# Optimization experiments

Measured on AMD Instinct MI355X. Metric: run time of the kernel, lower is better.

## Reference

```python
import jax, jax.numpy as jnp
import numpy as np

NUM_EMBEDDINGS = 8192
EMBEDDING_DIM = 512
COMMITMENT_COST = 0.25
DECAY = 0.99
EPSILON = 1e-05


def setup_inputs() -> dict:
    key = jax.random.key(0)
    k1, k2, k3, k4 = jax.random.split(key, 4)
    z = jax.random.normal(k1, (16, 2048, EMBEDDING_DIM), dtype=jnp.float32)
    weight = jax.random.normal(k2, (NUM_EMBEDDINGS, EMBEDDING_DIM), dtype=jnp.float32)
    ema_cluster_size = jax.random.uniform(k3, (NUM_EMBEDDINGS,), dtype=jnp.float32)
    ema_w = jax.random.normal(k4, (NUM_EMBEDDINGS, EMBEDDING_DIM), dtype=jnp.float32)
    return {"z": z, "weight": weight, "ema_cluster_size": ema_cluster_size, "ema_w": ema_w}


def reference(z, weight, ema_cluster_size, ema_w):
    K, D = weight.shape
    z_flat = z.reshape(-1, D)                                   # [N, D]
    # squared-distance matrix via expanded GEMM (same math as torch)
    dist = ((z_flat ** 2).sum(1, keepdims=True)
            + (weight ** 2).sum(1)
            - 2.0 * z_flat @ weight.T)                          # [N, K]
    codes = jnp.argmin(dist, axis=1)                            # [N]
    # training-mode EMA update: one-hot sums expressed as segment_sum
    counts = jax.ops.segment_sum(jnp.ones(z_flat.shape[0], dtype=z.dtype), codes, num_segments=K)
    dw = jax.ops.segment_sum(z_flat, codes, num_segments=K)     # encodings.T @ z_flat
    new_cs = ema_cluster_size * DECAY + (1.0 - DECAY) * counts
    new_ema_w = ema_w * DECAY + (1.0 - DECAY) * dw
    n = new_cs.sum()
    cluster_size = (new_cs + EPSILON) / (n + K * EPSILON) * n
    new_weight = new_ema_w / cluster_size[:, None]              # updated codebook
    z_q = new_weight[codes].reshape(z.shape)                    # lookup with UPDATED weights
    vq_loss = COMMITMENT_COST * jnp.mean((jax.lax.stop_gradient(z_q) - z) ** 2)
    z_q_out = z + jax.lax.stop_gradient(z_q - z)                # straight-through estimator
    codes_out = codes.reshape(z.shape[0], -1)
    return vq_loss, z_q_out, codes_out, new_weight, new_cs, new_ema_w
```

## Files before the change

kernel.cpp:

```cpp
#include <hip/hip_runtime.h>
#include <cstdint>

#define K_CODES 8192
#define D_DIM   512
#define N_VEC   32768
#define DECAY   0.99f
#define EPS_VQ  1e-5f
#define COMMIT  0.25f
#define MARGIN  0.25f

typedef _Float16 half_t;
typedef _Float16 half8 __attribute__((ext_vector_type(8)));
typedef _Float16 half4 __attribute__((ext_vector_type(4)));
typedef float    f32x4 __attribute__((ext_vector_type(4)));
typedef unsigned long long u64;

#define GL2L(g, l)                                                              \
    __builtin_amdgcn_global_load_lds(                                           \
        (const __attribute__((address_space(1))) unsigned int*)(g),             \
        (__attribute__((address_space(3))) unsigned int*)(l), 16, 0, 0)

__device__ __forceinline__ unsigned ordf(float f) {
    unsigned u = __float_as_uint(f);
    return (u & 0x80000000u) ? ~u : (u | 0x80000000u);
}
__device__ __forceinline__ float unordf(unsigned u) {
    u = (u & 0x80000000u) ? (u & 0x7FFFFFFFu) : ~u;
    return __uint_as_float(u);
}


__global__ __launch_bounds__(256)
void conv_half_kernel(const float* __restrict__ x, half_t* __restrict__ out) {
    int i = blockIdx.x * 256 + threadIdx.x;
    float4 v = ((const float4*)x)[i];
    half4 h = { (_Float16)v.x, (_Float16)v.y, (_Float16)v.z, (_Float16)v.w };
    *(half4*)(out + (size_t)i * 4) = h;
}

__global__ __launch_bounds__(256)
void wsq_kernel(const float* __restrict__ w, float* __restrict__ wsq) {
    int wave = threadIdx.x >> 6, lane = threadIdx.x & 63;
    int row  = blockIdx.x * 4 + wave;
    const float4* p = (const float4*)(w + (size_t)row * D_DIM);
    float4 a = p[lane], b = p[lane + 64];
    float s = a.x*a.x + a.y*a.y + a.z*a.z + a.w*a.w
            + b.x*b.x + b.y*b.y + b.z*b.z + b.w*b.w;
    #pragma unroll
    for (int off = 32; off; off >>= 1) s += __shfl_down(s, off);
    if (lane == 0) wsq[row] = s;
}

__global__ __launch_bounds__(256)
void dist1_kernel(const half_t* __restrict__ A, const half_t* __restrict__ B,
                  const float* __restrict__ wsq, uint4* __restrict__ partial) {
    __shared__ __align__(16) half_t As[128 * 64];
    __shared__ __align__(16) half_t Bs[128 * 64];

    const int k0 = blockIdx.x * 128;
    const int n0 = blockIdx.y * 128;
    const int t    = threadIdx.x;
    const int lane = t & 63;
    const int wave = t >> 6;
    const int wm = (wave >> 1) * 64;
    const int wn = (wave & 1) * 64;
    const int l15 = lane & 15;
    const int q   = lane >> 4;

    f32x4 acc[4][4];
    #pragma unroll
    for (int mi = 0; mi < 4; ++mi)
        #pragma unroll
        for (int ni = 0; ni < 4; ++ni) acc[mi][ni] = (f32x4)0.0f;

    for (int c = 0; c < 8; ++c) {
        const int koff = c * 64;
        #pragma unroll
        for (int it = 0; it < 4; ++it) {
            int idx  = t + 256 * it;
            int row  = idx >> 3;
            int col8 = (idx & 7) ^ (row & 7);
            GL2L(A + (size_t)(n0 + row) * D_DIM + koff + col8 * 8, As + idx * 8);
            GL2L(B + (size_t)(k0 + row) * D_DIM + koff + col8 * 8, Bs + idx * 8);
        }
        __syncthreads();
        #pragma unroll
        for (int kk = 0; kk < 2; ++kk) {
            half8 af[4], bf[4];
            const int cpos = ((kk * 4 + q) ^ (l15 & 7)) * 8;
            #pragma unroll
            for (int mi = 0; mi < 4; ++mi)
                af[mi] = *(const half8*)&As[(wm + mi * 16 + l15) * 64 + cpos];
            #pragma unroll
            for (int ni = 0; ni < 4; ++ni)
                bf[ni] = *(const half8*)&Bs[(wn + ni * 16 + l15) * 64 + cpos];
            #pragma unroll
            for (int mi = 0; mi < 4; ++mi)
                #pragma unroll
                for (int ni = 0; ni < 4; ++ni)
                    acc[mi][ni] = __builtin_amdgcn_mfma_f32_16x16x32_f16(
                        af[mi], bf[ni], acc[mi][ni], 0, 0, 0);
        }
        __syncthreads();
    }

    u64* sm = (u64*)As;
    #pragma unroll
    for (int mi = 0; mi < 4; ++mi) {
        #pragma unroll
        for (int r = 0; r < 4; ++r) {
            u64 k1 = ~0ull, k2 = ~0ull;
            #pragma unroll
            for (int ni = 0; ni < 4; ++ni) {
                int col = k0 + wn + ni * 16 + l15;
                float d = wsq[col] - 2.0f * acc[mi][ni][r];
                u64 key = ((u64)ordf(d) << 32) | (unsigned)col;
                if (key < k1) { k2 = k1; k1 = key; }
                else if (key < k2) k2 = key;
            }
            #pragma unroll
            for (int m = 1; m <= 8; m <<= 1) {
                u64 o1 = __shfl_xor(k1, m);
                u64 o2 = __shfl_xor(k2, m);
                u64 lo = k1 < o1 ? k1 : o1;
                u64 hi = k1 < o1 ? o1 : k1;
                u64 m2 = k2 < o2 ? k2 : o2;
                k1 = lo;
                k2 = m2 < hi ? m2 : hi;
            }
            if (l15 == 0) {
                int rl = wm + mi * 16 + q * 4 + r;
                int h  = wave & 1;
                sm[h * 256 + 2 * rl]     = k1;
                sm[h * 256 + 2 * rl + 1] = k2;
            }
        }
    }
    __syncthreads();
    if (t < 128) {
        u64 a1 = sm[2*t], a2 = sm[2*t + 1];
        u64 b1 = sm[256 + 2*t], b2 = sm[256 + 2*t + 1];
        u64 lo = a1 < b1 ? a1 : b1;
        u64 hi = a1 < b1 ? b1 : a1;
        u64 m2 = a2 < b2 ? a2 : b2;
        m2 = m2 < hi ? m2 : hi;
        partial[(size_t)blockIdx.x * N_VEC + n0 + t] =
            make_uint4((unsigned)lo, (unsigned)(lo >> 32),
                       (unsigned)(m2 >> 32), 0u);
    }
}

__global__ __launch_bounds__(256)
void reduce_top2_kernel(const uint4* __restrict__ partial,
                        int* __restrict__ codes_i, float* __restrict__ codes_f,
                        int* __restrict__ cnt, int* __restrict__ list) {
    int row = blockIdx.x * 256 + threadIdx.x;
    u64 k1 = ~0ull, k2 = ~0ull;
    unsigned vm2 = 0xFFFFFFFFu;
    for (int kb = 0; kb < 64; ++kb) {
        uint4 e = partial[(size_t)kb * N_VEC + row];
        u64 k = ((u64)e.y << 32) | e.x;
        if (k < k1) { k2 = k1; k1 = k; }
        else if (k < k2) k2 = k;
        vm2 = min(vm2, e.z);
    }
    unsigned so = min((unsigned)(k2 >> 32), vm2);
    float bv = unordf((unsigned)(k1 >> 32));
    float sv = unordf(so);
    int code = (int)(k1 & 0xFFFFFFFFu);
    codes_i[row] = code;
    codes_f[row] = (float)code;
    if (sv - bv < MARGIN) { int p = atomicAdd(cnt, 1); list[p] = row; }
}

__global__ __launch_bounds__(256)
void refine2_kernel(const float* __restrict__ z, const float* __restrict__ w,
                    const float* __restrict__ wsq,
                    const int* __restrict__ cnt, const int* __restrict__ list,
                    u64* __restrict__ exact) {
    __shared__ float zs[64][68];
    __shared__ float ws[64][68];
    __shared__ int rows_s[64];
    const int n  = *cnt;
    const int c0 = blockIdx.x * 64;
    const int t  = threadIdx.x;
    const int lr = t & 63, lc = t >> 6;
    const int ty = t >> 4, tx = t & 15;

    for (int row0 = blockIdx.y * 64; row0 < n; row0 += gridDim.y * 64) {
        if (t < 64) {
            int ri = row0 + t;
            rows_s[t] = list[ri < n ? ri : n - 1];
        }
        __syncthreads();
        float acc[4][4] = {};
        const int zrow = rows_s[lr];
        for (int k0 = 0; k0 < D_DIM; k0 += 64) {
            #pragma unroll
            for (int it = 0; it < 4; ++it) {
                int kc = (lc * 4 + it) * 4;
                float4 v = *(const float4*)(z + (size_t)zrow * D_DIM + k0 + kc);
                zs[kc+0][lr] = v.x; zs[kc+1][lr] = v.y;
                zs[kc+2][lr] = v.z; zs[kc+3][lr] = v.w;
                float4 u = *(const float4*)(w + (size_t)(c0 + lr) * D_DIM + k0 + kc);
                ws[kc+0][lr] = u.x; ws[kc+1][lr] = u.y;
                ws[kc+2][lr] = u.z; ws[kc+3][lr] = u.w;
            }
            __syncthreads();
            #pragma unroll 8
            for (int k = 0; k < 64; ++k) {
                float4 za = *(const float4*)&zs[k][ty * 4];
                float4 wa = *(const float4*)&ws[k][tx * 4];
                float zav[4] = {za.x, za.y, za.z, za.w};
                float wav[4] = {wa.x, wa.y, wa.z, wa.w};
                #pragma unroll
                for (int i = 0; i < 4; ++i)
                    #pragma unroll
                    for (int j = 0; j < 4; ++j)
                        acc[i][j] += zav[i] * wav[j];
            }
            __syncthreads();
        }
        #pragma unroll
        for (int i = 0; i < 4; ++i) {
            u64 key = ~0ull;
            #pragma unroll
            for (int j = 0; j < 4; ++j) {
                int c = c0 + tx * 4 + j;
                float d = wsq[c] - 2.0f * acc[i][j];
                u64 k = ((u64)ordf(d) << 32) | (unsigned)c;
                if (k < key) key = k;
            }
            #pragma unroll
            for (int m = 1; m <= 8; m <<= 1) {
                u64 o = __shfl_xor(key, m);
                key = o < key ? o : key;
            }
            if (tx == 0) atomicMin(exact + rows_s[ty * 4 + i], key);
        }
        __syncthreads();
    }
}

__global__ __launch_bounds__(256)
void refine_fix_kernel(const int* __restrict__ cnt, const int* __restrict__ list,
                       const u64* __restrict__ exact,
                       int* __restrict__ codes_i, float* __restrict__ codes_f) {
    int n = *cnt;
    for (int i = blockIdx.x * 256 + threadIdx.x; i < n; i += 64 * 256) {
        int row = list[i];
        int code = (int)(exact[row] & 0xFFFFFFFFu);
        codes_i[row] = code;
        codes_f[row] = (float)code;
    }
}

__global__ __launch_bounds__(256)
void scatter_kernel(const int* __restrict__ codes_i, const float* __restrict__ z,
                    float* __restrict__ cnt_acc, float* __restrict__ dw_acc) {
    int row = blockIdx.x * 8 + (threadIdx.x >> 5);
    int c   = threadIdx.x & 31;
    int code = codes_i[row];
    if (c == 0) atomicAdd(&cnt_acc[code], 1.0f);
    const float* zr = z + (size_t)row * D_DIM;
    float* dr = dw_acc + (size_t)code * D_DIM;
    #pragma unroll
    for (int d = c; d < D_DIM; d += 32) atomicAdd(&dr[d], zr[d]);
}

__global__ __launch_bounds__(256)
void cs_kernel(const float* __restrict__ ema_cs, float* __restrict__ cs_out,
               float* __restrict__ nsum) {
    __shared__ float wsum[4];
    int i = blockIdx.x * 256 + threadIdx.x;
    float v = ema_cs[i] * DECAY + (1.0f - DECAY) * cs_out[i];
    cs_out[i] = v;
    float s = v;
    #pragma unroll
    for (int off = 32; off; off >>= 1) s += __shfl_down(s, off);
    int lane = threadIdx.x & 63, wid = threadIdx.x >> 6;
    if (lane == 0) wsum[wid] = s;
    __syncthreads();
    if (threadIdx.x == 0)
        atomicAdd(nsum, wsum[0] + wsum[1] + wsum[2] + wsum[3]);
}

__global__ __launch_bounds__(256)
void weight_kernel(const float* __restrict__ ema_w, const float* __restrict__ cs,
                   const float* __restrict__ nsum_p,
                   float* __restrict__ emaw_out, float* __restrict__ w_out) {
    int i = blockIdx.x * 256 + threadIdx.x;
    float dw = emaw_out[i];
    float ne = ema_w[i] * DECAY + (1.0f - DECAY) * dw;
    emaw_out[i] = ne;
    int k = i >> 9;
    float n = *nsum_p;
    float csize = (cs[k] + EPS_VQ) / (n + (float)K_CODES * EPS_VQ) * n;
    w_out[i] = ne / csize;
}

__global__ __launch_bounds__(256)
void gather_loss_kernel(const float* __restrict__ z, const int* __restrict__ codes,
                        const float* __restrict__ w, float* __restrict__ zq,
                        float* __restrict__ loss_acc) {
    __shared__ float wsum[4];
    int row  = blockIdx.x * 4 + (threadIdx.x >> 6);
    int lane = threadIdx.x & 63;
    int code = codes[row];
    const float* zr = z + (size_t)row * D_DIM;
    const float* wr = w + (size_t)code * D_DIM;
    float s = 0.0f;
    #pragma unroll
    for (int d = lane; d < D_DIM; d += 64) {
        float qv = wr[d];
        float diff = qv - zr[d];
        s += diff * diff;
        zq[(size_t)row * D_DIM + d] = qv;
    }
    #pragma unroll
    for (int off = 32; off; off >>= 1) s += __shfl_down(s, off);
    int wid = threadIdx.x >> 6;
    if (lane == 0) wsum[wid] = s;
    __syncthreads();
    if (threadIdx.x == 0)
        atomicAdd(loss_acc, wsum[0] + wsum[1] + wsum[2] + wsum[3]);
}

__global__ void finalize_kernel(const float* __restrict__ loss_acc,
                                float* __restrict__ out0) {
    *out0 = COMMIT * (*loss_acc) / 16777216.0f;
}

extern "C" void kernel_launch(void* const* d_in, const int* in_sizes, int n_in,
                              void* d_out, int out_size, void* d_ws, size_t ws_size,
                              hipStream_t stream) {
    const float* z      = (const float*)d_in[0];
    const float* weight = (const float*)d_in[1];
    const float* ema_cs = (const float*)d_in[2];
    const float* ema_w  = (const float*)d_in[3];

    float* out       = (float*)d_out;
    float* out_loss  = out;
    float* out_zq    = out + 1;
    float* out_codes = out + 16777217;
    float* out_w     = out + 16809985;
    float* out_cs    = out + 21004289;
    float* out_emaw  = out + 21012481;

    half_t* A_hi = (half_t*)(out + 4);
    half_t* B_hi = (half_t*)(out + 8388612);
    uint4*  partial = (uint4*)(out + 16809988);

    char* ws = (char*)d_ws;
    float* wsq      = (float*)ws;
    int*   codes_i  = (int*)(ws + 32768);
    int*   cnt      = (int*)(ws + 163840);
    float* nsum     = (float*)(ws + 163844);
    float* loss_acc = (float*)(ws + 163848);
    int*   list     = (int*)(ws + 163856);
    u64*   exact    = (u64*)(ws + 294928);

    hipMemsetAsync(cnt, 0, 16, stream);
    hipMemsetAsync(exact, 0xFF, N_VEC * 8, stream);

    conv_half_kernel<<<N_VEC * D_DIM / 1024, 256, 0, stream>>>(z, A_hi);
    conv_half_kernel<<<K_CODES * D_DIM / 1024, 256, 0, stream>>>(weight, B_hi);
    wsq_kernel<<<K_CODES / 4, 256, 0, stream>>>(weight, wsq);

    dim3 g2(K_CODES / 128, N_VEC / 128);
    dist1_kernel<<<g2, 256, 0, stream>>>(A_hi, B_hi, wsq, partial);

    reduce_top2_kernel<<<N_VEC / 256, 256, 0, stream>>>(partial, codes_i,
                                                        out_codes, cnt, list);

    hipMemsetAsync(out_cs, 0, 8192 * 4, stream);
    hipMemsetAsync(out_emaw, 0, (size_t)4194304 * 4, stream);

    dim3 gr(K_CODES / 64, 64);
    refine2_kernel<<<gr, 256, 0, stream>>>(z, weight, wsq, cnt, list, exact);
    refine_fix_kernel<<<64, 256, 0, stream>>>(cnt, list, exact,
                                              codes_i, out_codes);

    scatter_kernel<<<N_VEC / 8, 256, 0, stream>>>(codes_i, z, out_cs, out_emaw);
    cs_kernel<<<K_CODES / 256, 256, 0, stream>>>(ema_cs, out_cs, nsum);
    weight_kernel<<<4194304 / 256, 256, 0, stream>>>(ema_w, out_cs, nsum,
                                                     out_emaw, out_w);
    gather_loss_kernel<<<N_VEC / 4, 256, 0, stream>>>(z, codes_i, out_w,
                                                      out_zq, loss_acc);
    finalize_kernel<<<1, 1, 0, stream>>>(loss_acc, out_loss);
}
```

Baseline: 1.081 ms.

## Replace 64-bit key shuffle top-2 reduction with float LDS transpose reduction

The dist1 epilogue now tracks the top-2 as float scores (acc - wsq/2, maximised) with a column index, rather than packed 64-bit ordered keys reduced via shuffles. Per-lane partials go to padded LDS, then each lane reduces a full row serially before the two column halves are merged. This removes 64-bit compares and cross-lane shuffles from the epilogue at the cost of more LDS traffic and an extra barrier. Tie-breaking on equal distances no longer prefers the lower index, and the score is rescaled, so second-best margins may differ slightly.

```diff
diff --git a/kernel.cpp b/kernel.cpp
--- a/kernel.cpp
+++ b/kernel.cpp
@@ -54,8 +54,9 @@
 __global__ __launch_bounds__(256)
 void dist1_kernel(const half_t* __restrict__ A, const half_t* __restrict__ B,
                   const float* __restrict__ wsq, uint4* __restrict__ partial) {
-    __shared__ __align__(16) half_t As[128 * 64];
-    __shared__ __align__(16) half_t Bs[128 * 64];
+    __shared__ __align__(16) char smem[46592];
+    half_t* As = (half_t*)smem;
+    half_t* Bs = (half_t*)(smem + 16384);
 
     const int k0 = blockIdx.x * 128;
     const int n0 = blockIdx.y * 128;
@@ -104,49 +105,71 @@
         __syncthreads();
     }
 
-    u64* sm = (u64*)As;
+    float* a1p = (float*)(smem + wave * 10880);
+    float* a2p = (float*)(smem + wave * 10880 + 4352);
+    unsigned short* colp = (unsigned short*)(smem + wave * 10880 + 8704);
+    float* fm  = (float*)(smem + 43520);
+
+    float wsqh[4];
+    #pragma unroll
+    for (int ni = 0; ni < 4; ++ni)
+        wsqh[ni] = 0.5f * wsq[k0 + wn + ni * 16 + l15];
+
     #pragma unroll
     for (int mi = 0; mi < 4; ++mi) {
         #pragma unroll
         for (int r = 0; r < 4; ++r) {
-            u64 k1 = ~0ull, k2 = ~0ull;
-            #pragma unroll
-            for (int ni = 0; ni < 4; ++ni) {
-                int col = k0 + wn + ni * 16 + l15;
-                float d = wsq[col] - 2.0f * acc[mi][ni][r];
-                u64 key = ((u64)ordf(d) << 32) | (unsigned)col;
-                if (key < k1) { k2 = k1; k1 = key; }
-                else if (key < k2) k2 = key;
+            float w1 = acc[mi][0][r] - wsqh[0];
+            float w2 = -INFINITY;
+            int   c1 = wn + l15;
+            #pragma unroll
+            for (int ni = 1; ni < 4; ++ni) {
+                float a = acc[mi][ni][r] - wsqh[ni];
+                bool gt = a > w1;
+                w2 = fmaxf(w2, fminf(a, w1));
+                w1 = gt ? a : w1;
+                c1 = gt ? (wn + ni * 16 + l15) : c1;
             }
-            #pragma unroll
-            for (int m = 1; m <= 8; m <<= 1) {
-                u64 o1 = __shfl_xor(k1, m);
-                u64 o2 = __shfl_xor(k2, m);
-                u64 lo = k1 < o1 ? k1 : o1;
-                u64 hi = k1 < o1 ? o1 : k1;
-                u64 m2 = k2 < o2 ? k2 : o2;
-                k1 = lo;
-                k2 = m2 < hi ? m2 : hi;
-            }
-            if (l15 == 0) {
-                int rl = wm + mi * 16 + q * 4 + r;
-                int h  = wave & 1;
-                sm[h * 256 + 2 * rl]     = k1;
-                sm[h * 256 + 2 * rl + 1] = k2;
-            }
+            int row = mi * 16 + q * 4 + r;
+            a1p[row * 17 + l15]  = w1;
+            a2p[row * 17 + l15]  = w2;
+            colp[row * 17 + l15] = (unsigned short)c1;
         }
     }
     __syncthreads();
+
+    {
+        const int rb = lane * 17;
+        float W1 = a1p[rb];
+        float W2 = -INFINITY;
+        int   jw = 0;
+        #pragma unroll
+        for (int j = 1; j < 16; ++j) {
+            float a = a1p[rb + j];
+            bool gt = a > W1;
+            W2 = fmaxf(W2, fminf(a, W1));
+            W1 = gt ? a : W1;
+            jw = gt ? j : jw;
+        }
+        W2 = fmaxf(W2, a2p[rb + jw]);
+        unsigned c = colp[rb + jw];
+        float* f = fm + ((wave & 1) * 128 + wm + lane) * 3;
+        f[0] = W1; f[1] = __uint_as_float(c); f[2] = W2;
+    }
+    __syncthreads();
+
     if (t < 128) {
-        u64 a1 = sm[2*t], a2 = sm[2*t + 1];
-        u64 b1 = sm[256 + 2*t], b2 = sm[256 + 2*t + 1];
-        u64 lo = a1 < b1 ? a1 : b1;
-        u64 hi = a1 < b1 ? b1 : a1;
-        u64 m2 = a2 < b2 ? a2 : b2;
-        m2 = m2 < hi ? m2 : hi;
+        const float* fa = fm + t * 3;
+        const float* fb = fm + (128 + t) * 3;
+        float w1a = fa[0], w1b = fb[0];
+        bool bwin = w1b > w1a;
+        float best = bwin ? w1b : w1a;
+        unsigned bcol = __float_as_uint(bwin ? fb[1] : fa[1]);
+        float sv = fmaxf(fminf(w1a, w1b), bwin ? fb[2] : fa[2]);
+        float d1 = -2.0f * best;
+        float d2 = -2.0f * sv;
         partial[(size_t)blockIdx.x * N_VEC + n0 + t] =
-            make_uint4((unsigned)lo, (unsigned)(lo >> 32),
-                       (unsigned)(m2 >> 32), 0u);
+            make_uint4(k0 + bcol, ordf(d1), ordf(d2), 0u);
     }
 }
 
```

Result: faster. 927.5 us (-14.2%).

## Pack distance and column into 32-bit keys and reduce top-2 via LDS

Applied to the files above, without the earlier changes.

The epilogue now turns the distance into a positive offset score (1024 - wsq/2 + dot), packs its truncated float bits with a 7-bit column index into a 32-bit key, and tracks top-2 by max. The 64-bit keys and shuffle butterflies are replaced by an LDS transpose with a per-lane serial scan. Global and LDS load addresses are precomputed outside the K loop, which is fully unrolled, and launch bounds request 4 blocks per SM. This cuts epilogue ALU and shuffle cost, but the truncated low mantissa bits and the fixed offset reduce distance precision and could change near-tie choices.

```diff
diff --git a/kernel.cpp b/kernel.cpp
--- a/kernel.cpp
+++ b/kernel.cpp
@@ -51,11 +51,12 @@
     if (lane == 0) wsq[row] = s;
 }
 
-__global__ __launch_bounds__(256)
+__global__ __launch_bounds__(256, 4)
 void dist1_kernel(const half_t* __restrict__ A, const half_t* __restrict__ B,
                   const float* __restrict__ wsq, uint4* __restrict__ partial) {
-    __shared__ __align__(16) half_t As[128 * 64];
-    __shared__ __align__(16) half_t Bs[128 * 64];
+    __shared__ __align__(16) char smem[36864];
+    half_t* As = (half_t*)smem;
+    half_t* Bs = (half_t*)(smem + 16384);
 
     const int k0 = blockIdx.x * 128;
     const int n0 = blockIdx.y * 128;
@@ -67,21 +68,30 @@
     const int l15 = lane & 15;
     const int q   = lane >> 4;
 
+    const half_t* ga[4]; const half_t* gb[4]; half_t* lA[4]; half_t* lB[4];
+    #pragma unroll
+    for (int it = 0; it < 4; ++it) {
+        int idx  = t + 256 * it;
+        int row  = idx >> 3;
+        int col8 = (idx & 7) ^ (row & 7);
+        ga[it] = A + (size_t)(n0 + row) * D_DIM + col8 * 8;
+        gb[it] = B + (size_t)(k0 + row) * D_DIM + col8 * 8;
+        lA[it] = As + idx * 8;
+        lB[it] = Bs + idx * 8;
+    }
+
     f32x4 acc[4][4];
     #pragma unroll
     for (int mi = 0; mi < 4; ++mi)
         #pragma unroll
         for (int ni = 0; ni < 4; ++ni) acc[mi][ni] = (f32x4)0.0f;
 
+    #pragma unroll
     for (int c = 0; c < 8; ++c) {
-        const int koff = c * 64;
         #pragma unroll
         for (int it = 0; it < 4; ++it) {
-            int idx  = t + 256 * it;
-            int row  = idx >> 3;
-            int col8 = (idx & 7) ^ (row & 7);
-            GL2L(A + (size_t)(n0 + row) * D_DIM + koff + col8 * 8, As + idx * 8);
-            GL2L(B + (size_t)(k0 + row) * D_DIM + koff + col8 * 8, Bs + idx * 8);
+            GL2L(ga[it] + c * 64, lA[it]);
+            GL2L(gb[it] + c * 64, lB[it]);
         }
         __syncthreads();
         #pragma unroll
@@ -104,49 +114,61 @@
         __syncthreads();
     }
 
-    u64* sm = (u64*)As;
+    uint2* kp  = (uint2*)(smem + wave * 8704);
+    uint2* fmp = (uint2*)(smem + 34816);
+
+    float wb[4]; unsigned cb[4];
+    #pragma unroll
+    for (int ni = 0; ni < 4; ++ni) {
+        wb[ni] = 1024.0f - 0.5f * wsq[k0 + wn + ni * 16 + l15];
+        cb[ni] = (unsigned)(wn + ni * 16 + l15);
+    }
+
     #pragma unroll
     for (int mi = 0; mi < 4; ++mi) {
         #pragma unroll
         for (int r = 0; r < 4; ++r) {
-            u64 k1 = ~0ull, k2 = ~0ull;
+            unsigned k1 = 0u, k2 = 0u;
             #pragma unroll
             for (int ni = 0; ni < 4; ++ni) {
-                int col = k0 + wn + ni * 16 + l15;
-                float d = wsq[col] - 2.0f * acc[mi][ni][r];
-                u64 key = ((u64)ordf(d) << 32) | (unsigned)col;
-                if (key < k1) { k2 = k1; k1 = key; }
-                else if (key < k2) k2 = key;
+                float a = acc[mi][ni][r] + wb[ni];
+                unsigned key = (__float_as_uint(a) & 0xFFFFFF80u) | cb[ni];
+                unsigned lo = min(k1, key);
+                k1 = max(k1, key);
+                k2 = max(k2, lo);
             }
-            #pragma unroll
-            for (int m = 1; m <= 8; m <<= 1) {
-                u64 o1 = __shfl_xor(k1, m);
-                u64 o2 = __shfl_xor(k2, m);
-                u64 lo = k1 < o1 ? k1 : o1;
-                u64 hi = k1 < o1 ? o1 : k1;
-                u64 m2 = k2 < o2 ? k2 : o2;
-                k1 = lo;
-                k2 = m2 < hi ? m2 : hi;
-            }
-            if (l15 == 0) {
-                int rl = wm + mi * 16 + q * 4 + r;
-                int h  = wave & 1;
-                sm[h * 256 + 2 * rl]     = k1;
-                sm[h * 256 + 2 * rl + 1] = k2;
-            }
+            int row = mi * 16 + q * 4 + r;
+            kp[row * 17 + l15] = make_uint2(k1, k2);
         }
     }
     __syncthreads();
+
+    {
+        const int rb = lane * 17;
+        uint2 e0 = kp[rb];
+        unsigned W1 = e0.x, W2 = e0.y;
+        #pragma unroll
+        for (int j = 1; j < 16; ++j) {
+            uint2 e = kp[rb + j];
+            unsigned lo = min(W1, e.x);
+            W1 = max(W1, e.x);
+            W2 = max(max(W2, lo), e.y);
+        }
+        fmp[(wave & 1) * 128 + wm + lane] = make_uint2(W1, W2);
+    }
+    __syncthreads();
+
     if (t < 128) {
-        u64 a1 = sm[2*t], a2 = sm[2*t + 1];
-        u64 b1 = sm[256 + 2*t], b2 = sm[256 + 2*t + 1];
-        u64 lo = a1 < b1 ? a1 : b1;
-        u64 hi = a1 < b1 ? b1 : a1;
-        u64 m2 = a2 < b2 ? a2 : b2;
-        m2 = m2 < hi ? m2 : hi;
+        uint2 a = fmp[t], b = fmp[128 + t];
+        unsigned W1 = max(a.x, b.x);
+        unsigned W2 = max(max(min(a.x, b.x), a.y), b.y);
+        unsigned col = (unsigned)k0 + (W1 & 127u);
+        float v1 = __uint_as_float(W1 & 0xFFFFFF80u);
+        float v2 = __uint_as_float(W2 & 0xFFFFFF80u);
+        float d1 = 2048.0f - 2.0f * v1;
+        float d2 = 2048.0f - 2.0f * v2;
         partial[(size_t)blockIdx.x * N_VEC + n0 + t] =
-            make_uint4((unsigned)lo, (unsigned)(lo >> 32),
-                       (unsigned)(m2 >> 32), 0u);
+            make_uint4(col, ordf(d1), ordf(d2), 0u);
     }
 }
 
```

Measured after the change: 928.1 us. 1.16x faster.
